# Optimization experiments

Hardware: AMD Instinct MI355X
Metric: run time of the kernel (lower is better)

## Reference

```python
import jax, jax.numpy as jnp
import numpy as np

BH, N, D, M = 64, 8192, 64, 32


def _gaussian_orthogonal_random_matrix(nb_rows, nb_cols, rng):
    # faithful to torch version with scaling=0: QR-orthogonal rows scaled by
    # row norms of a gaussian matrix
    blocks = []
    rows_left = nb_rows
    while rows_left > 0:
        q, _ = np.linalg.qr(rng.standard_normal((nb_cols, nb_cols)))
        blocks.append(q.T[: min(rows_left, nb_cols)])
        rows_left -= nb_cols
    final = np.concatenate(blocks, axis=0)[:nb_rows]
    multiplier = np.linalg.norm(rng.standard_normal((nb_rows, nb_cols)), axis=1)
    return (multiplier[:, None] * final).astype(np.float32)


def setup_inputs() -> dict:
    key = jax.random.key(0)
    k1, k2, k3 = jax.random.split(key, 3)
    q = jax.random.normal(k1, (BH, N, D), dtype=jnp.float32)
    k = jax.random.normal(k2, (BH, N, D), dtype=jnp.float32)
    v = jax.random.normal(k3, (BH, N, D), dtype=jnp.float32)
    proj = jnp.asarray(_gaussian_orthogonal_random_matrix(M, D, np.random.default_rng(0)))
    return {"q": q, "k": k, "v": v, "proj": proj}


def _softmax_kernel(data, proj, is_query, eps=1e-4):
    d = data.shape[-1]
    data_normalizer = d ** -0.25
    ratio = proj.shape[0] ** -0.5
    # [bh, n, m] random-feature logits
    data_dash = jnp.einsum('bnd,md->bnm', data_normalizer * data, proj)
    diag = (0.5 * data_normalizer ** 2) * jnp.sum(data * data, axis=-1, keepdims=True)
    if is_query:
        mx = jnp.max(data_dash, axis=-1, keepdims=True)  # per-row max
    else:
        mx = jnp.max(data_dash)  # global max (as in torch.max(t) with no dim)
    return ratio * (jnp.exp(data_dash - diag - mx) + eps)


def reference(q, k, v, proj):
    qp = _softmax_kernel(q, proj, is_query=True)   # [bh, n, m]
    kp = _softmax_kernel(k, proj, is_query=False)  # [bh, n, m]
    # linear attention: k^T v aggregation then query contraction
    kv = jnp.einsum('bnm,bnd->bmd', kp, v)         # [bh, m, d]
    ksum = jnp.sum(kp, axis=1)                     # [bh, m]
    num = jnp.einsum('bnm,bmd->bnd', qp, kv)       # [bh, n, d]
    den = jnp.einsum('bnm,bm->bn', qp, ksum)       # [bh, n]
    return num / den[..., None]
```

## Files before the change

kernel.cpp:

```cpp
#include <hip/hip_runtime.h>
#include <math.h>

#define BH 64
#define NN 8192
#define DD 64
#define MM 32

#define NROWS (BH*NN)
#define NORMC 0.35355339059327379f
#define RATIO 0.17677669529663689f
#define EPSK  1e-4f
#define DIAGC 0.0625f

#define CPB 32
#define CHUNK 256
#define K12_BLOCKS (BH*CPB)

typedef __attribute__((ext_vector_type(8))) short short8;
typedef __attribute__((ext_vector_type(4))) float f32x4;

union FragU { uint4 u; short8 s; };

__device__ __forceinline__ unsigned bf16r(float x) {
  unsigned u = __float_as_uint(x);
  return (u + 0x7fffu + ((u >> 16) & 1u)) >> 16;
}
__device__ __forceinline__ void cvt8(const float* f, FragU& hi, FragU& lo) {
  unsigned h[8], lw[8];
  #pragma unroll
  for (int j = 0; j < 8; ++j) {
    h[j] = bf16r(f[j]);
    lw[j] = bf16r(f[j] - __uint_as_float(h[j] << 16));
  }
  hi.u = make_uint4(h[0]|(h[1]<<16),  h[2]|(h[3]<<16),  h[4]|(h[5]<<16),  h[6]|(h[7]<<16));
  lo.u = make_uint4(lw[0]|(lw[1]<<16), lw[2]|(lw[3]<<16), lw[4]|(lw[5]<<16), lw[6]|(lw[7]<<16));
}

#define MFMA(a,b,c) __builtin_amdgcn_mfma_f32_16x16x32_bf16((a),(b),(c),0,0,0)

__device__ __forceinline__ float wave_max(float v) {
  #pragma unroll
  for (int off = 32; off > 0; off >>= 1)
    v = fmaxf(v, __shfl_down(v, off, 64));
  return v;
}

__global__ void kfrag_proj(const float* __restrict__ proj,
                           uint4* __restrict__ pfH, uint4* __restrict__ pfL)
{
  const int t = threadIdx.x;
  const int l = t & 63, g = t >> 6;
  const int mt = g >> 1, ks = g & 1;
  const int lr = l & 15, lg = l >> 4;
  float f[8];
  #pragma unroll
  for (int j = 0; j < 8; ++j)
    f[j] = proj[(mt*16 + lr)*DD + ks*32 + lg*8 + j];
  FragU hi, lo; cvt8(f, hi, lo);
  pfH[g*64 + l] = hi.u;
  pfL[g*64 + l] = lo.u;
}

__global__ __launch_bounds__(256, 3) void k12_kv(
    const float* __restrict__ k, const float* __restrict__ v,
    const uint4* __restrict__ pfH, const uint4* __restrict__ pfL,
    float* __restrict__ kvPart, float* __restrict__ ksPart,
    float* __restrict__ vsPart, float* __restrict__ partialMax)
{
  __shared__ float red[8192];
  __shared__ float wmaxL[4];
  const int t = threadIdx.x;
  const int w = t >> 6, l = t & 63;
  const int lr = l & 15, lg = l >> 4;
  const int blk = blockIdx.x;
  const int b = blk >> 5, c = blk & (CPB - 1);
  const size_t gbase = (size_t)b * NN + (size_t)c * CHUNK + (size_t)w * 64;

  ushort* eh = (ushort*)red + w * 2560;
  ushort* el = eh + 1280;

  f32x4 accK[2][4];
  #pragma unroll
  for (int mt = 0; mt < 2; ++mt)
    #pragma unroll
    for (int dt = 0; dt < 4; ++dt)
      accK[mt][dt] = (f32x4){0.f, 0.f, 0.f, 0.f};
  float ksacc0 = 0.f, ksacc1 = 0.f;
  float vsum[4] = {0.f, 0.f, 0.f, 0.f};
  float tmax = -3.4e38f;

  for (int nb = 0; nb < 2; ++nb) {
    const size_t nrow0 = gbase + nb * 32;

    #pragma unroll
    for (int rt = 0; rt < 2; ++rt) {
      float sq = 0.f;
      f32x4 a0 = {0.f,0.f,0.f,0.f}, a1 = {0.f,0.f,0.f,0.f};
      #pragma unroll
      for (int ks = 0; ks < 2; ++ks) {
        const float4* src = (const float4*)(k + (nrow0 + rt*16 + lr)*DD + ks*32 + lg*8);
        float4 x0 = src[0], x1 = src[1];
        float qv[8] = {x0.x,x0.y,x0.z,x0.w, x1.x,x1.y,x1.z,x1.w};
        #pragma unroll
        for (int j = 0; j < 8; ++j) sq += qv[j]*qv[j];
        FragU aH, aL; cvt8(qv, aH, aL);

        uintptr_t pfh_ = (uintptr_t)pfH, pfl_ = (uintptr_t)pfL;
        asm volatile("" : "+s"(pfh_), "+s"(pfl_));
        const uint4* pH = (const uint4*)pfh_;
        const uint4* pL = (const uint4*)pfl_;
        FragU pH0, pH1, pL0, pL1;
        pH0.u = pH[ks*64 + l];
        pH1.u = pH[(2+ks)*64 + l];
        pL0.u = pL[ks*64 + l];
        pL1.u = pL[(2+ks)*64 + l];

        a0 = MFMA(aL.s, pH0.s, a0);
        a0 = MFMA(aH.s, pL0.s, a0);
        a0 = MFMA(aH.s, pH0.s, a0);
        a1 = MFMA(aL.s, pH1.s, a1);
        a1 = MFMA(aH.s, pL1.s, a1);
        a1 = MFMA(aH.s, pH1.s, a1);
      }
      sq += __shfl_xor(sq, 16, 64);
      sq += __shfl_xor(sq, 32, 64);
      unsigned h0w[4], l0w[4], h1w[4], l1w[4];
      #pragma unroll
      for (int reg = 0; reg < 4; ++reg) {
        const float diag = DIAGC * __shfl(sq, lg*4 + reg, 64);
        const float d0 = a0[reg] * NORMC;
        const float d1 = a1[reg] * NORMC;
        tmax = fmaxf(tmax, fmaxf(d0, d1));
        const float e0 = __expf(d0 - diag);
        const float e1 = __expf(d1 - diag);
        ksacc0 += e0;
        ksacc1 += e1;
        h0w[reg] = bf16r(e0);
        l0w[reg] = bf16r(e0 - __uint_as_float(h0w[reg] << 16));
        h1w[reg] = bf16r(e1);
        l1w[reg] = bf16r(e1 - __uint_as_float(h1w[reg] << 16));
      }
      const int nloc = rt*16 + lg*4;
      *(unsigned*)(eh + lr*40      + nloc)     = h0w[0] | (h0w[1] << 16);
      *(unsigned*)(eh + lr*40      + nloc + 2) = h0w[2] | (h0w[3] << 16);
      *(unsigned*)(el + lr*40      + nloc)     = l0w[0] | (l0w[1] << 16);
      *(unsigned*)(el + lr*40      + nloc + 2) = l0w[2] | (l0w[3] << 16);
      *(unsigned*)(eh + (lr+16)*40 + nloc)     = h1w[0] | (h1w[1] << 16);
      *(unsigned*)(eh + (lr+16)*40 + nloc + 2) = h1w[2] | (h1w[3] << 16);
      *(unsigned*)(el + (lr+16)*40 + nloc)     = l1w[0] | (l1w[1] << 16);
      *(unsigned*)(el + (lr+16)*40 + nloc + 2) = l1w[2] | (l1w[3] << 16);
    }

    #pragma unroll
    for (int dt = 0; dt < 4; ++dt) {
      float vv[8];
      #pragma unroll
      for (int j = 0; j < 8; ++j)
        vv[j] = v[(nrow0 + lg*8 + j)*DD + dt*16 + lr];
      vsum[dt] += vv[0]+vv[1]+vv[2]+vv[3]+vv[4]+vv[5]+vv[6]+vv[7];
      FragU bHv, bLv; cvt8(vv, bHv, bLv);
      #pragma unroll
      for (int mt = 0; mt < 2; ++mt) {
        FragU aHk, aLk;
        aHk.u = *(const uint4*)(eh + (mt*16 + lr)*40 + lg*8);
        aLk.u = *(const uint4*)(el + (mt*16 + lr)*40 + lg*8);
        accK[mt][dt] = MFMA(aLk.s, bHv.s, accK[mt][dt]);
        accK[mt][dt] = MFMA(aHk.s, bLv.s, accK[mt][dt]);
        accK[mt][dt] = MFMA(aHk.s, bHv.s, accK[mt][dt]);
      }
    }
  }

  tmax = wave_max(tmax);
  if (l == 0) wmaxL[w] = tmax;
  ksacc0 += __shfl_xor(ksacc0, 16, 64);
  ksacc0 += __shfl_xor(ksacc0, 32, 64);
  ksacc1 += __shfl_xor(ksacc1, 16, 64);
  ksacc1 += __shfl_xor(ksacc1, 32, 64);
  #pragma unroll
  for (int dt = 0; dt < 4; ++dt) {
    vsum[dt] += __shfl_xor(vsum[dt], 16, 64);
    vsum[dt] += __shfl_xor(vsum[dt], 32, 64);
  }
  __syncthreads();
  #pragma unroll
  for (int mt = 0; mt < 2; ++mt)
    #pragma unroll
    for (int dt = 0; dt < 4; ++dt)
      #pragma unroll
      for (int reg = 0; reg < 4; ++reg)
        red[((mt*16 + lg*4 + reg)*64 + dt*16 + lr)*4 + w] = accK[mt][dt][reg];
  __syncthreads();
  if (t == 0)
    partialMax[blk] = fmaxf(fmaxf(wmaxL[0], wmaxL[1]), fmaxf(wmaxL[2], wmaxL[3]));
  #pragma unroll
  for (int ii = 0; ii < 8; ++ii) {
    const int o = t + 256 * ii;
    const float4 r4 = *(const float4*)&red[o*4];
    kvPart[(size_t)blk * 2048 + o] = r4.x + r4.y + r4.z + r4.w;
  }
  __syncthreads();
  if (l < 16) {
    red[w*32 + lr]        = ksacc0;
    red[w*32 + 16 + lr]   = ksacc1;
    #pragma unroll
    for (int dt = 0; dt < 4; ++dt)
      red[128 + w*64 + dt*16 + lr] = vsum[dt];
  }
  __syncthreads();
  if (t < 32)
    ksPart[blk*32 + t] = red[t] + red[32+t] + red[64+t] + red[96+t];
  if (t < 64)
    vsPart[blk*64 + t] = red[128+t] + red[192+t] + red[256+t] + red[320+t];
}

__global__ __launch_bounds__(256) void k1b_reduce_max(
    const float* __restrict__ partialMax, float* __restrict__ gmax)
{
  const int t = threadIdx.x;
  float mx = -3.4e38f;
  for (int i = t; i < K12_BLOCKS; i += 256) mx = fmaxf(mx, partialMax[i]);
  mx = wave_max(mx);
  __shared__ float wmaxs[4];
  if ((t & 63) == 0) wmaxs[t >> 6] = mx;
  __syncthreads();
  if (t == 0)
    *gmax = fmaxf(fmaxf(wmaxs[0], wmaxs[1]), fmaxf(wmaxs[2], wmaxs[3]));
}

__global__ __launch_bounds__(256) void k2b_reduce(
    const float* __restrict__ kvPart, const float* __restrict__ ksPart,
    const float* __restrict__ vsPart, const float* __restrict__ gmaxPtr,
    float* __restrict__ ksF, uint4* __restrict__ kfH, uint4* __restrict__ kfL)
{
  __shared__ float vsumL[64];
  __shared__ float kvL[2048];
  const int b = blockIdx.x, t = threadIdx.x;
  const float scale = __expf(-*gmaxPtr);
  if (t < 64) {
    float s = 0.f;
    for (int c = 0; c < CPB; ++c)
      s += vsPart[(b * CPB + c) * 64 + t];
    vsumL[t] = s;
  }
  __syncthreads();
  #pragma unroll
  for (int ii = 0; ii < 8; ++ii) {
    const int o = t + 256 * ii;
    float s = 0.f;
    for (int c = 0; c < CPB; ++c)
      s += kvPart[((size_t)(b * CPB + c)) * 2048 + o];
    kvL[o] = RATIO * (scale * s + EPSK * vsumL[o & 63]);
  }
  if (t < 32) {
    float s = 0.f;
    for (int c = 0; c < CPB; ++c)
      s += ksPart[(b * CPB + c) * 32 + t];
    ksF[b * 32 + t] = RATIO * (scale * s + EPSK * (float)NN);
  }
  __syncthreads();
  {
    const int l = t & 63, dt = t >> 6;
    const int lr = l & 15, lg = l >> 4;
    float f[8];
    #pragma unroll
    for (int j = 0; j < 8; ++j)
      f[j] = kvL[(lg*8 + j)*64 + dt*16 + lr];
    FragU hi, lo; cvt8(f, hi, lo);
    kfH[(b*4 + dt)*64 + l] = hi.u;
    kfL[(b*4 + dt)*64 + l] = lo.u;
  }
}

__global__ __launch_bounds__(256, 4) void k3_out(
    const float* __restrict__ q,
    const uint4* __restrict__ pfH, const uint4* __restrict__ pfL,
    const uint4* __restrict__ kfH, const uint4* __restrict__ kfL,
    const float* __restrict__ ksF, float* __restrict__ out)
{
  __shared__ float dashL[256][36];
  __shared__ float ssqL[256][4];
  const int t = threadIdx.x;
  const int w = t >> 6, l = t & 63;
  const int lr = l & 15, lg = l >> 4;
  const int b = blockIdx.x >> 5;
  const size_t rowBase = (size_t)blockIdx.x * 256;
  const int wrb = w * 64;

  FragU pbH[2][2], pbL[2][2];
  #pragma unroll
  for (int mt = 0; mt < 2; ++mt)
    #pragma unroll
    for (int ks = 0; ks < 2; ++ks) {
      pbH[mt][ks].u = pfH[(mt*2+ks)*64 + l];
      pbL[mt][ks].u = pfL[(mt*2+ks)*64 + l];
    }

  #pragma unroll
  for (int rt = 0; rt < 4; ++rt) {
    const int rrow = wrb + rt*16 + lr;
    f32x4 acc0 = {0.f,0.f,0.f,0.f}, acc1 = {0.f,0.f,0.f,0.f};
    float sq = 0.f;
    #pragma unroll
    for (int ks = 0; ks < 2; ++ks) {
      const float4* src = (const float4*)(q + (rowBase + rrow)*DD + ks*32 + lg*8);
      float4 a0 = src[0], a1 = src[1];
      float qv[8] = {a0.x,a0.y,a0.z,a0.w, a1.x,a1.y,a1.z,a1.w};
      #pragma unroll
      for (int j = 0; j < 8; ++j) sq += qv[j]*qv[j];
      FragU aH, aL; cvt8(qv, aH, aL);
      acc0 = MFMA(aL.s, pbH[0][ks].s, acc0);
      acc0 = MFMA(aH.s, pbL[0][ks].s, acc0);
      acc0 = MFMA(aH.s, pbH[0][ks].s, acc0);
      acc1 = MFMA(aL.s, pbH[1][ks].s, acc1);
      acc1 = MFMA(aH.s, pbL[1][ks].s, acc1);
      acc1 = MFMA(aH.s, pbH[1][ks].s, acc1);
    }
    ssqL[rrow][lg] = sq;
    #pragma unroll
    for (int reg = 0; reg < 4; ++reg) {
      dashL[wrb + rt*16 + lg*4 + reg][lr]      = acc0[reg];
      dashL[wrb + rt*16 + lg*4 + reg][16 + lr] = acc1[reg];
    }
  }

  {
    float dv[32];
    const float4* dr = (const float4*)&dashL[t][0];
    #pragma unroll
    for (int i = 0; i < 8; ++i) {
      float4 v4 = dr[i];
      dv[4*i]=v4.x; dv[4*i+1]=v4.y; dv[4*i+2]=v4.z; dv[4*i+3]=v4.w;
    }
    const float ssq = ssqL[t][0]+ssqL[t][1]+ssqL[t][2]+ssqL[t][3];
    float mx = -3.4e38f;
    #pragma unroll
    for (int m = 0; m < MM; ++m) { dv[m] *= NORMC; mx = fmaxf(mx, dv[m]); }
    const float sub = DIAGC * ssq + mx;
    const float* __restrict__ ksb = ksF + b * 32;
    float den = 0.f;
    #pragma unroll
    for (int m = 0; m < MM; ++m) {
      dv[m] = RATIO * (__expf(dv[m] - sub) + EPSK);
      den = fmaf(dv[m], ksb[m], den);
    }
    const float inv = 1.0f / den;
    unsigned hiw[16], low[16];
    #pragma unroll
    for (int u = 0; u < 16; ++u) {
      const float x0 = dv[2*u] * inv, x1 = dv[2*u+1] * inv;
      const unsigned h0 = bf16r(x0);
      const unsigned l0 = bf16r(x0 - __uint_as_float(h0 << 16));
      const unsigned h1 = bf16r(x1);
      const unsigned l1 = bf16r(x1 - __uint_as_float(h1 << 16));
      hiw[u] = h0 | (h1 << 16);
      low[u] = l0 | (l1 << 16);
    }
    uint4* pr = (uint4*)&dashL[t][0];
    pr[0] = make_uint4(hiw[0],hiw[1],hiw[2],hiw[3]);
    pr[1] = make_uint4(hiw[4],hiw[5],hiw[6],hiw[7]);
    pr[2] = make_uint4(hiw[8],hiw[9],hiw[10],hiw[11]);
    pr[3] = make_uint4(hiw[12],hiw[13],hiw[14],hiw[15]);
    pr[4] = make_uint4(low[0],low[1],low[2],low[3]);
    pr[5] = make_uint4(low[4],low[5],low[6],low[7]);
    pr[6] = make_uint4(low[8],low[9],low[10],low[11]);
    pr[7] = make_uint4(low[12],low[13],low[14],low[15]);
  }

  FragU kbH[4], kbL[4];
  #pragma unroll
  for (int dt = 0; dt < 4; ++dt) {
    kbH[dt].u = kfH[(b*4 + dt)*64 + l];
    kbL[dt].u = kfL[(b*4 + dt)*64 + l];
  }
  #pragma unroll
  for (int rt = 0; rt < 4; ++rt) {
    const uint4* pr = (const uint4*)&dashL[wrb + rt*16 + lr][0];
    FragU aH, aL;
    aH.u = pr[lg];
    aL.u = pr[4 + lg];
    #pragma unroll
    for (int dt = 0; dt < 4; ++dt) {
      f32x4 o = {0.f,0.f,0.f,0.f};
      o = MFMA(aL.s, kbH[dt].s, o);
      o = MFMA(aH.s, kbL[dt].s, o);
      o = MFMA(aH.s, kbH[dt].s, o);
      float* ob = out + (rowBase + wrb + rt*16 + lg*4)*DD + dt*16 + lr;
      ob[0]      = o[0];
      ob[DD]     = o[1];
      ob[2*DD]   = o[2];
      ob[3*DD]   = o[3];
    }
  }
}

extern "C" void kernel_launch(void* const* d_in, const int* in_sizes, int n_in,
                              void* d_out, int out_size, void* d_ws, size_t ws_size,
                              hipStream_t stream) {
  const float* q    = (const float*)d_in[0];
  const float* k    = (const float*)d_in[1];
  const float* v    = (const float*)d_in[2];
  const float* proj = (const float*)d_in[3];
  float* out = (float*)d_out;
  float* ws  = (float*)d_ws;

  float*    partialMax = ws;
  float*    gmax       = ws + 2048;
  float*    kvPart     = ws + 4096;
  float*    ksPart     = kvPart + 4194304;
  float*    vsPart     = ksPart + 65536;
  float*    ksF        = vsPart + 131072;
  unsigned* pfH        = (unsigned*)(ksF + 2048);
  unsigned* pfL        = pfH + 1024;
  unsigned* kfH        = pfL + 1024;
  unsigned* kfL        = kfH + 65536;

  kfrag_proj<<<1, 256, 0, stream>>>(proj, (uint4*)pfH, (uint4*)pfL);
  k12_kv<<<K12_BLOCKS, 256, 0, stream>>>(k, v, (uint4*)pfH, (uint4*)pfL,
                                         kvPart, ksPart, vsPart, partialMax);
  k1b_reduce_max<<<1, 256, 0, stream>>>(partialMax, gmax);
  k2b_reduce<<<BH, 256, 0, stream>>>(kvPart, ksPart, vsPart, gmax,
                                     ksF, (uint4*)kfH, (uint4*)kfL);
  k3_out<<<NROWS / 256, 256, 0, stream>>>(q, (uint4*)pfH, (uint4*)pfL,
                                          (uint4*)kfH, (uint4*)kfL, ksF, out);
}
```

Baseline: 149.8 us.

## Use one wave per k12 block, each processing the whole chunk

The k12_kv kernel now runs one 64-thread wave per block, and that wave loops over all 256 rows of the chunk instead of splitting them across four waves. The shared-memory cross-wave reduction and its barriers go away, and each wave writes its partial kv, ksum, vsum and max directly to global memory. The trade-off is less parallelism per chunk: 2048 single-wave blocks run longer serial loops, which can lower occupancy and leave latency hidden only through more resident blocks.

```diff
diff --git a/kernel.cpp b/kernel.cpp
--- a/kernel.cpp
+++ b/kernel.cpp
@@ -61,23 +61,19 @@
   pfL[g*64 + l] = lo.u;
 }
 
-__global__ __launch_bounds__(256, 3) void k12_kv(
+__global__ __launch_bounds__(64, 4) void k12_kv(
     const float* __restrict__ k, const float* __restrict__ v,
     const uint4* __restrict__ pfH, const uint4* __restrict__ pfL,
     float* __restrict__ kvPart, float* __restrict__ ksPart,
     float* __restrict__ vsPart, float* __restrict__ partialMax)
 {
-  __shared__ float red[8192];
-  __shared__ float wmaxL[4];
-  const int t = threadIdx.x;
-  const int w = t >> 6, l = t & 63;
+  __shared__ ushort eh[1280];
+  __shared__ ushort el[1280];
+  const int l = threadIdx.x;
   const int lr = l & 15, lg = l >> 4;
   const int blk = blockIdx.x;
   const int b = blk >> 5, c = blk & (CPB - 1);
-  const size_t gbase = (size_t)b * NN + (size_t)c * CHUNK + (size_t)w * 64;
-
-  ushort* eh = (ushort*)red + w * 2560;
-  ushort* el = eh + 1280;
+  const size_t gbase = (size_t)b * NN + (size_t)c * CHUNK;
 
   f32x4 accK[2][4];
   #pragma unroll
@@ -89,7 +85,7 @@
   float vsum[4] = {0.f, 0.f, 0.f, 0.f};
   float tmax = -3.4e38f;
 
-  for (int nb = 0; nb < 2; ++nb) {
+  for (int nb = 0; nb < CHUNK / 32; ++nb) {
     const size_t nrow0 = gbase + nb * 32;
 
     #pragma unroll
@@ -172,7 +168,7 @@
   }
 
   tmax = wave_max(tmax);
-  if (l == 0) wmaxL[w] = tmax;
+  if (l == 0) partialMax[blk] = tmax;
   ksacc0 += __shfl_xor(ksacc0, 16, 64);
   ksacc0 += __shfl_xor(ksacc0, 32, 64);
   ksacc1 += __shfl_xor(ksacc1, 16, 64);
@@ -182,36 +178,21 @@
     vsum[dt] += __shfl_xor(vsum[dt], 16, 64);
     vsum[dt] += __shfl_xor(vsum[dt], 32, 64);
   }
-  __syncthreads();
+  float* kvp = kvPart + (size_t)blk * 2048;
   #pragma unroll
   for (int mt = 0; mt < 2; ++mt)
     #pragma unroll
     for (int dt = 0; dt < 4; ++dt)
       #pragma unroll
       for (int reg = 0; reg < 4; ++reg)
-        red[((mt*16 + lg*4 + reg)*64 + dt*16 + lr)*4 + w] = accK[mt][dt][reg];
-  __syncthreads();
-  if (t == 0)
-    partialMax[blk] = fmaxf(fmaxf(wmaxL[0], wmaxL[1]), fmaxf(wmaxL[2], wmaxL[3]));
-  #pragma unroll
-  for (int ii = 0; ii < 8; ++ii) {
-    const int o = t + 256 * ii;
-    const float4 r4 = *(const float4*)&red[o*4];
-    kvPart[(size_t)blk * 2048 + o] = r4.x + r4.y + r4.z + r4.w;
-  }
-  __syncthreads();
-  if (l < 16) {
-    red[w*32 + lr]        = ksacc0;
-    red[w*32 + 16 + lr]   = ksacc1;
+        kvp[(mt*16 + lg*4 + reg)*64 + dt*16 + lr] = accK[mt][dt][reg];
+  if (lg == 0) {
+    ksPart[blk*32 + lr]      = ksacc0;
+    ksPart[blk*32 + 16 + lr] = ksacc1;
     #pragma unroll
     for (int dt = 0; dt < 4; ++dt)
-      red[128 + w*64 + dt*16 + lr] = vsum[dt];
-  }
-  __syncthreads();
-  if (t < 32)
-    ksPart[blk*32 + t] = red[t] + red[32+t] + red[64+t] + red[96+t];
-  if (t < 64)
-    vsPart[blk*64 + t] = red[128+t] + red[192+t] + red[256+t] + red[320+t];
+      vsPart[blk*64 + dt*16 + lr] = vsum[dt];
+  }
 }
 
 __global__ __launch_bounds__(256) void k1b_reduce_max(
@@ -416,8 +397,8 @@
   unsigned* kfL        = kfH + 65536;
 
   kfrag_proj<<<1, 256, 0, stream>>>(proj, (uint4*)pfH, (uint4*)pfL);
-  k12_kv<<<K12_BLOCKS, 256, 0, stream>>>(k, v, (uint4*)pfH, (uint4*)pfL,
-                                         kvPart, ksPart, vsPart, partialMax);
+  k12_kv<<<K12_BLOCKS, 64, 0, stream>>>(k, v, (uint4*)pfH, (uint4*)pfL,
+                                        kvPart, ksPart, vsPart, partialMax);
   k1b_reduce_max<<<1, 256, 0, stream>>>(partialMax, gmax);
   k2b_reduce<<<BH, 256, 0, stream>>>(kvPart, ksPart, vsPart, gmax,
                                      ksF, (uint4*)kfH, (uint4*)kfL);
```

Result: slower. 182.5 us (+21.8%).
